# Optimization experiments

Hardware: AMD Instinct MI355X
Metric: run time of the kernel (lower is better)

The kernel has to match this reference:

```python
import jax, jax.numpy as jnp
import numpy as np

B, T, N, C, K = 32, 16, 512, 128, 2


def setup_inputs() -> dict:
    key = jax.random.key(0)
    k1, k2, k3 = jax.random.split(key, 3)
    x = jax.random.normal(k1, (B, T, N, C), dtype=jnp.float32)
    adj = jax.random.uniform(k2, (B, N, N), dtype=jnp.float32)
    lambdas = jnp.ones((K,), dtype=jnp.float32)           # raw lambda params (init 1.0)
    thetas = jax.random.uniform(k3, (K, C, C), dtype=jnp.float32)  # torch.rand init
    return {"x": x, "adj": adj, "lambdas": lambdas, "thetas": thetas}


def _akgcn_layer(x, adj, lam_raw, theta):
    # x: [B,T,N,C], adj: [B,N,N]
    lam = 1.0 + jax.nn.relu(lam_raw)  # actual lambda
    h = jnp.einsum('btnc,cd->btnd', x, theta)
    eye = jnp.eye(adj.shape[-1], dtype=adj.dtype)
    v = ((2.0 * lam - 2.0) / lam) * eye + (2.0 / lam) * adj   # [B,N,N]
    v = v / jnp.sum(v, axis=-1, keepdims=True)                 # row-normalize
    out = jnp.einsum('bnm,btmd->btnd', v, h)                   # vectorized over T
    return jax.nn.relu(out)


def reference(x, adj, lambdas, thetas):
    hid = x
    for k in range(K):  # small fixed layer count
        hid = _akgcn_layer(hid, adj, lambdas[k], thetas[k])
    return jax.nn.relu(x) + jax.nn.sigmoid(hid)
```

## Files before the change

kernel.cpp:

```cpp
#include <hip/hip_runtime.h>
#include <hip/hip_bf16.h>

#define BB 32
#define TT 16
#define NNODE 512
#define CC 128

typedef __attribute__((ext_vector_type(8))) short bf16x8;
typedef __attribute__((ext_vector_type(4))) short short4_t;
typedef __attribute__((ext_vector_type(4))) float f32x4;

__device__ __forceinline__ short f2bf(float f) {
    __hip_bfloat16 h = __float2bfloat16(f);
    return *reinterpret_cast<short*>(&h);
}

#define GLD16(g, l)                                                          \
    __builtin_amdgcn_global_load_lds(                                        \
        (const __attribute__((address_space(1))) unsigned int*)(g),          \
        (__attribute__((address_space(3))) unsigned int*)(l), 16, 0, 0)

__global__ void prep_adj2_kernel(const float* __restrict__ adj,
                                 const float* __restrict__ lambdas, int layer,
                                 short* __restrict__ Abf) {
    int gid = blockIdx.x * blockDim.x + threadIdx.x;
    int row = gid >> 6;
    int lane = gid & 63;
    int n = row & (NNODE - 1);
    const float* r = adj + (long)row * NNODE;
    float4 f0 = *(const float4*)(r + lane * 4);
    float4 f1 = *(const float4*)(r + 256 + lane * 4);
    float s = f0.x + f0.y + f0.z + f0.w + f1.x + f1.y + f1.z + f1.w;
#pragma unroll
    for (int o = 32; o; o >>= 1) s += __shfl_xor(s, o, 64);
    float lamm1 = fmaxf(lambdas[layer], 0.f);
    float inv = 1.f / (s + lamm1);
    float v[8] = {f0.x, f0.y, f0.z, f0.w, f1.x, f1.y, f1.z, f1.w};
#pragma unroll
    for (int j = 0; j < 8; ++j) v[j] *= inv;
    int d0 = n - lane * 4;
    if (d0 >= 0 && d0 < 4) v[d0] += lamm1 * inv;
    int d1 = n - 256 - lane * 4;
    if (d1 >= 0 && d1 < 4) v[4 + d1] += lamm1 * inv;
    short* o = Abf + (long)row * NNODE;
    short4_t s0 = {f2bf(v[0]), f2bf(v[1]), f2bf(v[2]), f2bf(v[3])};
    short4_t s1 = {f2bf(v[4]), f2bf(v[5]), f2bf(v[6]), f2bf(v[7])};
    *(short4_t*)(o + lane * 4) = s0;
    *(short4_t*)(o + 256 + lane * 4) = s1;
}

__global__ void prep_theta_kernel(const float* __restrict__ theta,
                                  short* __restrict__ thT) {
    int idx = blockIdx.x * 256 + threadIdx.x;
    int i = idx >> 7, k = idx & (CC - 1);
    thT[i * CC + k] = f2bf(theta[k * CC + i]);
}

__global__ __launch_bounds__(256) void gemm_theta_mfma(
    const float* __restrict__ X, const short* __restrict__ thT,
    short* __restrict__ Ht) {
    __shared__ short As[128 * 32];
    __shared__ short Bs[128 * 32];
    const int t = threadIdx.x;
    const long rowBase = (long)blockIdx.x * 128;
    const int w = t >> 6, ln = t & 63;
    const int lm = ln & 15, q = ln >> 4;
    const int wy = w >> 1, wx = w & 1;

    f32x4 acc[4][4] = {};

    const int rr = w * 32 + (ln >> 2);
    const int kc = (ln & 3) * 8;
    short* ldsB = Bs + w * 1024 + ln * 8;

    for (int k0 = 0; k0 < CC; k0 += 32) {
        __syncthreads();
        const short* gb = thT + rr * CC + k0 + kc;
        GLD16(gb, ldsB);
        GLD16(gb + 16 * CC, ldsB + 512);
#pragma unroll
        for (int i = 0; i < 4; ++i) {
            int v = i * 256 + t;
            int r = v >> 3, kq = v & 7;
            float4 f = *(const float4*)(X + (rowBase + r) * CC + k0 + kq * 4);
            short4_t s = {f2bf(f.x), f2bf(f.y), f2bf(f.z), f2bf(f.w)};
            *(short4_t*)(&As[r * 32 + kq * 4]) = s;
        }
        __syncthreads();

        bf16x8 a[4], b[4];
#pragma unroll
        for (int i = 0; i < 4; ++i)
            a[i] = *(const bf16x8*)(&As[(wy * 64 + i * 16 + lm) * 32 + q * 8]);
#pragma unroll
        for (int j = 0; j < 4; ++j)
            b[j] = *(const bf16x8*)(&Bs[(wx * 64 + j * 16 + lm) * 32 + q * 8]);
#pragma unroll
        for (int i = 0; i < 4; ++i)
#pragma unroll
            for (int j = 0; j < 4; ++j)
                acc[i][j] = __builtin_amdgcn_mfma_f32_16x16x32_bf16(
                    a[i], b[j], acc[i][j], 0, 0, 0);
    }

    const long bt = rowBase >> 9;
    const int mBase = (int)(rowBase & (NNODE - 1));
    short* Hb = Ht + bt * (long)(NNODE * CC);
#pragma unroll
    for (int i = 0; i < 4; ++i) {
        int m = mBase + wy * 64 + i * 16 + q * 4;
#pragma unroll
        for (int j = 0; j < 4; ++j) {
            int c = wx * 64 + j * 16 + lm;
            f32x4 v = acc[i][j];
            short4_t s = {f2bf(v[0]), f2bf(v[1]), f2bf(v[2]), f2bf(v[3])};
            *(short4_t*)(&Hb[(long)c * NNODE + m]) = s;
        }
    }
}

__global__ __launch_bounds__(256) void gemm_agg_theta(
    const short* __restrict__ Abf, const short* __restrict__ Ht1,
    const short* __restrict__ thT2, short* __restrict__ Ht2) {
    __shared__ short As[128 * 32];
    __shared__ short Bs[128 * 32];
    __shared__ short Ts[128][136];
    const int t = threadIdx.x;
    const int bt = blockIdx.y;
    const int n0 = blockIdx.x * 128;
    const short* Ab = Abf + (long)(bt >> 4) * NNODE * NNODE + (long)n0 * NNODE;
    const short* Hb = Ht1 + (long)bt * NNODE * CC;
    const int w = t >> 6, ln = t & 63;
    const int lm = ln & 15, q = ln >> 4;
    const int wy = w >> 1, wx = w & 1;

    f32x4 acc[4][4] = {};

    const int rr = w * 32 + (ln >> 2);
    const int kc = (ln & 3) * 8;
    short* ldsA = As + w * 1024 + ln * 8;
    short* ldsB = Bs + w * 1024 + ln * 8;

    for (int k0 = 0; k0 < NNODE; k0 += 32) {
        __syncthreads();
        const short* ga = Ab + (long)rr * NNODE + k0 + kc;
        const short* gb = Hb + (long)rr * NNODE + k0 + kc;
        GLD16(ga, ldsA);
        GLD16(ga + 16 * NNODE, ldsA + 512);
        GLD16(gb, ldsB);
        GLD16(gb + 16 * NNODE, ldsB + 512);
        __syncthreads();

        bf16x8 a[4], b[4];
#pragma unroll
        for (int i = 0; i < 4; ++i)
            a[i] = *(const bf16x8*)(&As[(wy * 64 + i * 16 + lm) * 32 + q * 8]);
#pragma unroll
        for (int j = 0; j < 4; ++j)
            b[j] = *(const bf16x8*)(&Bs[(wx * 64 + j * 16 + lm) * 32 + q * 8]);
#pragma unroll
        for (int i = 0; i < 4; ++i)
#pragma unroll
            for (int j = 0; j < 4; ++j)
                acc[i][j] = __builtin_amdgcn_mfma_f32_16x16x32_bf16(
                    a[i], b[j], acc[i][j], 0, 0, 0);
    }

#pragma unroll
    for (int i = 0; i < 4; ++i)
#pragma unroll
        for (int j = 0; j < 4; ++j)
#pragma unroll
            for (int r = 0; r < 4; ++r)
                Ts[wy * 64 + i * 16 + q * 4 + r][wx * 64 + j * 16 + lm] =
                    f2bf(fmaxf(acc[i][j][r], 0.f));

    f32x4 acc2[4][4] = {};
    for (int c0 = 0; c0 < CC; c0 += 32) {
        __syncthreads();
        const short* gb = thT2 + rr * CC + c0 + kc;
        GLD16(gb, ldsB);
        GLD16(gb + 16 * CC, ldsB + 512);
        __syncthreads();

        bf16x8 a[4], b[4];
#pragma unroll
        for (int i = 0; i < 4; ++i)
            a[i] = *(const bf16x8*)(&Ts[wy * 64 + i * 16 + lm][c0 + q * 8]);
#pragma unroll
        for (int j = 0; j < 4; ++j)
            b[j] = *(const bf16x8*)(&Bs[(wx * 64 + j * 16 + lm) * 32 + q * 8]);
#pragma unroll
        for (int i = 0; i < 4; ++i)
#pragma unroll
            for (int j = 0; j < 4; ++j)
                acc2[i][j] = __builtin_amdgcn_mfma_f32_16x16x32_bf16(
                    a[i], b[j], acc2[i][j], 0, 0, 0);
    }

    short* Hb2 = Ht2 + (long)bt * NNODE * CC;
#pragma unroll
    for (int i = 0; i < 4; ++i) {
        int m = n0 + wy * 64 + i * 16 + q * 4;
#pragma unroll
        for (int j = 0; j < 4; ++j) {
            int c = wx * 64 + j * 16 + lm;
            f32x4 v = acc2[i][j];
            short4_t sv = {f2bf(v[0]), f2bf(v[1]), f2bf(v[2]), f2bf(v[3])};
            *(short4_t*)(&Hb2[(long)c * NNODE + m]) = sv;
        }
    }
}

template <int FUSE>
__global__ __launch_bounds__(256) void gemm_agg_mfma(
    const short* __restrict__ Abf, const short* __restrict__ Ht,
    const float* __restrict__ x, float* __restrict__ Out) {
    __shared__ short As[128 * 32];
    __shared__ short Bs[128 * 32];
    const int t = threadIdx.x;
    const int bt = blockIdx.y;
    const int n0 = blockIdx.x * 128;
    const short* Ab = Abf + (long)(bt >> 4) * NNODE * NNODE + (long)n0 * NNODE;
    const short* Hb = Ht + (long)bt * NNODE * CC;
    const int w = t >> 6, ln = t & 63;
    const int lm = ln & 15, q = ln >> 4;
    const int wy = w >> 1, wx = w & 1;

    f32x4 acc[4][4] = {};

    const int rr = w * 32 + (ln >> 2);
    const int kc = (ln & 3) * 8;
    short* ldsA = As + w * 1024 + ln * 8;
    short* ldsB = Bs + w * 1024 + ln * 8;

    for (int k0 = 0; k0 < NNODE; k0 += 32) {
        __syncthreads();
        const short* ga = Ab + (long)rr * NNODE + k0 + kc;
        const short* gb = Hb + (long)rr * NNODE + k0 + kc;
        GLD16(ga, ldsA);
        GLD16(ga + 16 * NNODE, ldsA + 512);
        GLD16(gb, ldsB);
        GLD16(gb + 16 * NNODE, ldsB + 512);
        __syncthreads();

        bf16x8 a[4], b[4];
#pragma unroll
        for (int i = 0; i < 4; ++i)
            a[i] = *(const bf16x8*)(&As[(wy * 64 + i * 16 + lm) * 32 + q * 8]);
#pragma unroll
        for (int j = 0; j < 4; ++j)
            b[j] = *(const bf16x8*)(&Bs[(wx * 64 + j * 16 + lm) * 32 + q * 8]);
#pragma unroll
        for (int i = 0; i < 4; ++i)
#pragma unroll
            for (int j = 0; j < 4; ++j)
                acc[i][j] = __builtin_amdgcn_mfma_f32_16x16x32_bf16(
                    a[i], b[j], acc[i][j], 0, 0, 0);
    }

    const long obase = (long)bt * NNODE * CC;
#pragma unroll
    for (int i = 0; i < 4; ++i) {
        int n = n0 + wy * 64 + i * 16 + q * 4;
#pragma unroll
        for (int j = 0; j < 4; ++j) {
            int c = wx * 64 + j * 16 + lm;
#pragma unroll
            for (int r = 0; r < 4; ++r) {
                long idx = obase + (long)(n + r) * CC + c;
                float v = fmaxf(acc[i][j][r], 0.f);
                if (FUSE) {
                    Out[idx] = fmaxf(x[idx], 0.f) + 1.f / (1.f + __expf(-v));
                } else {
                    Out[idx] = v;
                }
            }
        }
    }
}

extern "C" void kernel_launch(void* const* d_in, const int* in_sizes, int n_in,
                              void* d_out, int out_size, void* d_ws,
                              size_t ws_size, hipStream_t stream) {
    const float* x = (const float*)d_in[0];
    const float* adj = (const float*)d_in[1];
    const float* lambdas = (const float*)d_in[2];
    const float* thetas = (const float*)d_in[3];
    float* out = (float*)d_out;

    short* Abf = (short*)d_ws;
    short* Ht2 = Abf + (long)BB * NNODE * NNODE;
    short* thT0 = Ht2 + (long)BB * TT * NNODE * CC;
    short* thT1 = thT0 + CC * CC;
    short* Ht1 = (short*)out;

    dim3 blk(256);
    dim3 g_agg(NNODE / 128, BB * TT);

    prep_adj2_kernel<<<4096, blk, 0, stream>>>(adj, lambdas, 0, Abf);
    prep_theta_kernel<<<64, blk, 0, stream>>>(thetas, thT0);
    prep_theta_kernel<<<64, blk, 0, stream>>>(thetas + CC * CC, thT1);

    gemm_theta_mfma<<<2048, blk, 0, stream>>>(x, thT0, Ht1);

    gemm_agg_theta<<<g_agg, blk, 0, stream>>>(Abf, Ht1, thT1, Ht2);

    prep_adj2_kernel<<<4096, blk, 0, stream>>>(adj, lambdas, 1, Abf);
    gemm_agg_mfma<1><<<g_agg, blk, 0, stream>>>(Abf, Ht2, x, out);
}
```

Baseline: 434.1 us.

## Double-buffer aggregation GEMMs, remap blocks, fuse prep kernels and preload theta

The aggregation GEMMs now double-buffer their LDS tiles, issuing the next k-slice's global-to-LDS loads before the current MFMAs so that load latency overlaps compute. They also use a 1D grid with a swizzled block-to-tile mapping meant to improve L2 reuse of the shared adjacency rows. The adjacency prep computes both layers' normalized matrices in one pass when the workspace is large enough, and the two theta transposes are merged into one launch. The theta GEMM keeps the whole theta in LDS and converts X straight into registers, and the second GEMM in gemm_agg_theta reads theta from global memory instead of staging it. The costs are higher LDS and workspace use, and a fallback path for when the workspace is too small.

After: 504.0 us. 1.16x slower.

```diff
diff --git a/kernel.cpp b/kernel.cpp
--- a/kernel.cpp
+++ b/kernel.cpp
@@ -20,9 +20,10 @@
         (const __attribute__((address_space(1))) unsigned int*)(g),          \
         (__attribute__((address_space(3))) unsigned int*)(l), 16, 0, 0)
 
-__global__ void prep_adj2_kernel(const float* __restrict__ adj,
-                                 const float* __restrict__ lambdas, int layer,
-                                 short* __restrict__ Abf) {
+__global__ void prep_adj_kernel(const float* __restrict__ adj,
+                                const float* __restrict__ lambdas, int layer0,
+                                short* __restrict__ Abf0,
+                                short* __restrict__ Abf1) {
     int gid = blockIdx.x * blockDim.x + threadIdx.x;
     int row = gid >> 6;
     int lane = gid & 63;
@@ -33,68 +34,76 @@
     float s = f0.x + f0.y + f0.z + f0.w + f1.x + f1.y + f1.z + f1.w;
 #pragma unroll
     for (int o = 32; o; o >>= 1) s += __shfl_xor(s, o, 64);
-    float lamm1 = fmaxf(lambdas[layer], 0.f);
-    float inv = 1.f / (s + lamm1);
-    float v[8] = {f0.x, f0.y, f0.z, f0.w, f1.x, f1.y, f1.z, f1.w};
-#pragma unroll
-    for (int j = 0; j < 8; ++j) v[j] *= inv;
+    float base[8] = {f0.x, f0.y, f0.z, f0.w, f1.x, f1.y, f1.z, f1.w};
     int d0 = n - lane * 4;
-    if (d0 >= 0 && d0 < 4) v[d0] += lamm1 * inv;
     int d1 = n - 256 - lane * 4;
-    if (d1 >= 0 && d1 < 4) v[4 + d1] += lamm1 * inv;
-    short* o = Abf + (long)row * NNODE;
-    short4_t s0 = {f2bf(v[0]), f2bf(v[1]), f2bf(v[2]), f2bf(v[3])};
-    short4_t s1 = {f2bf(v[4]), f2bf(v[5]), f2bf(v[6]), f2bf(v[7])};
-    *(short4_t*)(o + lane * 4) = s0;
-    *(short4_t*)(o + 256 + lane * 4) = s1;
-}
-
-__global__ void prep_theta_kernel(const float* __restrict__ theta,
+#pragma unroll
+    for (int l = 0; l < 2; ++l) {
+        short* dst = l ? Abf1 : Abf0;
+        if (dst == nullptr) continue;
+        float lamm1 = fmaxf(lambdas[layer0 + l], 0.f);
+        float inv = 1.f / (s + lamm1);
+        float v[8];
+#pragma unroll
+        for (int j = 0; j < 8; ++j) v[j] = base[j] * inv;
+        if (d0 >= 0 && d0 < 4) v[d0] += lamm1 * inv;
+        if (d1 >= 0 && d1 < 4) v[4 + d1] += lamm1 * inv;
+        short* o = dst + (long)row * NNODE;
+        short4_t s0 = {f2bf(v[0]), f2bf(v[1]), f2bf(v[2]), f2bf(v[3])};
+        short4_t s1 = {f2bf(v[4]), f2bf(v[5]), f2bf(v[6]), f2bf(v[7])};
+        *(short4_t*)(o + lane * 4) = s0;
+        *(short4_t*)(o + 256 + lane * 4) = s1;
+    }
+}
+
+__global__ void prep_theta_kernel(const float* __restrict__ thetas,
                                   short* __restrict__ thT) {
     int idx = blockIdx.x * 256 + threadIdx.x;
-    int i = idx >> 7, k = idx & (CC - 1);
-    thT[i * CC + k] = f2bf(theta[k * CC + i]);
+    int l = idx >> 14;
+    int r = idx & 16383;
+    int i = r >> 7, k = r & (CC - 1);
+    thT[l * CC * CC + i * CC + k] = f2bf(thetas[l * CC * CC + k * CC + i]);
 }
 
 __global__ __launch_bounds__(256) void gemm_theta_mfma(
     const float* __restrict__ X, const short* __restrict__ thT,
     short* __restrict__ Ht) {
-    __shared__ short As[128 * 32];
-    __shared__ short Bs[128 * 32];
+    __shared__ short Bs[128][136];
     const int t = threadIdx.x;
     const long rowBase = (long)blockIdx.x * 128;
     const int w = t >> 6, ln = t & 63;
     const int lm = ln & 15, q = ln >> 4;
     const int wy = w >> 1, wx = w & 1;
 
+    {
+        int row = t >> 1, half = (t & 1) * 64;
+        const short* src = thT + row * CC + half;
+#pragma unroll
+        for (int j = 0; j < 8; ++j)
+            *(bf16x8*)(&Bs[row][half + j * 8]) = *(const bf16x8*)(src + j * 8);
+    }
+    __syncthreads();
+
     f32x4 acc[4][4] = {};
-
-    const int rr = w * 32 + (ln >> 2);
-    const int kc = (ln & 3) * 8;
-    short* ldsB = Bs + w * 1024 + ln * 8;
-
+    const float* Xr = X + (rowBase + wy * 64 + lm) * CC;
+#pragma unroll
     for (int k0 = 0; k0 < CC; k0 += 32) {
-        __syncthreads();
-        const short* gb = thT + rr * CC + k0 + kc;
-        GLD16(gb, ldsB);
-        GLD16(gb + 16 * CC, ldsB + 512);
+        bf16x8 a[4], b[4];
 #pragma unroll
         for (int i = 0; i < 4; ++i) {
-            int v = i * 256 + t;
-            int r = v >> 3, kq = v & 7;
-            float4 f = *(const float4*)(X + (rowBase + r) * CC + k0 + kq * 4);
-            short4_t s = {f2bf(f.x), f2bf(f.y), f2bf(f.z), f2bf(f.w)};
-            *(short4_t*)(&As[r * 32 + kq * 4]) = s;
-        }
-        __syncthreads();
-
-        bf16x8 a[4], b[4];
-#pragma unroll
-        for (int i = 0; i < 4; ++i)
-            a[i] = *(const bf16x8*)(&As[(wy * 64 + i * 16 + lm) * 32 + q * 8]);
-#pragma unroll
-        for (int j = 0; j < 4; ++j)
-            b[j] = *(const bf16x8*)(&Bs[(wx * 64 + j * 16 + lm) * 32 + q * 8]);
+            const float* p = Xr + i * 16 * CC + k0 + q * 8;
+            float4 g0 = *(const float4*)(p);
+            float4 g1 = *(const float4*)(p + 4);
+            bf16x8 av;
+            av[0] = f2bf(g0.x); av[1] = f2bf(g0.y);
+            av[2] = f2bf(g0.z); av[3] = f2bf(g0.w);
+            av[4] = f2bf(g1.x); av[5] = f2bf(g1.y);
+            av[6] = f2bf(g1.z); av[7] = f2bf(g1.w);
+            a[i] = av;
+        }
+#pragma unroll
+        for (int j = 0; j < 4; ++j)
+            b[j] = *(const bf16x8*)(&Bs[wx * 64 + j * 16 + lm][k0 + q * 8]);
 #pragma unroll
         for (int i = 0; i < 4; ++i)
 #pragma unroll
@@ -113,8 +122,8 @@
         for (int j = 0; j < 4; ++j) {
             int c = wx * 64 + j * 16 + lm;
             f32x4 v = acc[i][j];
-            short4_t s = {f2bf(v[0]), f2bf(v[1]), f2bf(v[2]), f2bf(v[3])};
-            *(short4_t*)(&Hb[(long)c * NNODE + m]) = s;
+            short4_t sv = {f2bf(v[0]), f2bf(v[1]), f2bf(v[2]), f2bf(v[3])};
+            *(short4_t*)(&Hb[(long)c * NNODE + m]) = sv;
         }
     }
 }
@@ -122,12 +131,12 @@
 __global__ __launch_bounds__(256) void gemm_agg_theta(
     const short* __restrict__ Abf, const short* __restrict__ Ht1,
     const short* __restrict__ thT2, short* __restrict__ Ht2) {
-    __shared__ short As[128 * 32];
-    __shared__ short Bs[128 * 32];
-    __shared__ short Ts[128][136];
+    __shared__ short sh[17408];
     const int t = threadIdx.x;
-    const int bt = blockIdx.y;
-    const int n0 = blockIdx.x * 128;
+    const int bid = blockIdx.x;
+    const int wid = (bid & 7) * 256 + (bid >> 3);
+    const int bt = wid >> 2;
+    const int n0 = (wid & 3) * 128;
     const short* Ab = Abf + (long)(bt >> 4) * NNODE * NNODE + (long)n0 * NNODE;
     const short* Hb = Ht1 + (long)bt * NNODE * CC;
     const int w = t >> 6, ln = t & 63;
@@ -138,58 +147,65 @@
 
     const int rr = w * 32 + (ln >> 2);
     const int kc = (ln & 3) * 8;
-    short* ldsA = As + w * 1024 + ln * 8;
-    short* ldsB = Bs + w * 1024 + ln * 8;
-
+    const short* ga = Ab + (long)rr * NNODE + kc;
+    const short* gb = Hb + (long)rr * NNODE + kc;
+    const int lofs = w * 1024 + ln * 8;
+
+    GLD16(ga, sh + lofs);
+    GLD16(ga + 16 * NNODE, sh + lofs + 512);
+    GLD16(gb, sh + 8192 + lofs);
+    GLD16(gb + 16 * NNODE, sh + 8192 + lofs + 512);
+    __syncthreads();
+    int sel = 0;
     for (int k0 = 0; k0 < NNODE; k0 += 32) {
-        __syncthreads();
-        const short* ga = Ab + (long)rr * NNODE + k0 + kc;
-        const short* gb = Hb + (long)rr * NNODE + k0 + kc;
-        GLD16(ga, ldsA);
-        GLD16(ga + 16 * NNODE, ldsA + 512);
-        GLD16(gb, ldsB);
-        GLD16(gb + 16 * NNODE, ldsB + 512);
-        __syncthreads();
-
+        if (k0 + 32 < NNODE) {
+            const int no = (sel ^ 1) * 4096 + lofs;
+            GLD16(ga + k0 + 32, sh + no);
+            GLD16(ga + k0 + 32 + 16 * NNODE, sh + no + 512);
+            GLD16(gb + k0 + 32, sh + 8192 + no);
+            GLD16(gb + k0 + 32 + 16 * NNODE, sh + 8192 + no + 512);
+        }
+        const short* Ac = sh + sel * 4096;
+        const short* Bc = sh + 8192 + sel * 4096;
         bf16x8 a[4], b[4];
 #pragma unroll
         for (int i = 0; i < 4; ++i)
-            a[i] = *(const bf16x8*)(&As[(wy * 64 + i * 16 + lm) * 32 + q * 8]);
-#pragma unroll
-        for (int j = 0; j < 4; ++j)
-            b[j] = *(const bf16x8*)(&Bs[(wx * 64 + j * 16 + lm) * 32 + q * 8]);
+            a[i] = *(const bf16x8*)(Ac + (wy * 64 + i * 16 + lm) * 32 + q * 8);
+#pragma unroll
+        for (int j = 0; j < 4; ++j)
+            b[j] = *(const bf16x8*)(Bc + (wx * 64 + j * 16 + lm) * 32 + q * 8);
 #pragma unroll
         for (int i = 0; i < 4; ++i)
 #pragma unroll
             for (int j = 0; j < 4; ++j)
                 acc[i][j] = __builtin_amdgcn_mfma_f32_16x16x32_bf16(
                     a[i], b[j], acc[i][j], 0, 0, 0);
-    }
-
+        __syncthreads();
+        sel ^= 1;
+    }
+
+    short(*Ts)[136] = (short(*)[136])sh;
 #pragma unroll
     for (int i = 0; i < 4; ++i)
 #pragma unroll
         for (int j = 0; j < 4; ++j)
 #pragma unroll
-            for (int r = 0; r < 4; ++r)
-                Ts[wy * 64 + i * 16 + q * 4 + r][wx * 64 + j * 16 + lm] =
-                    f2bf(fmaxf(acc[i][j][r], 0.f));
+            for (int r2 = 0; r2 < 4; ++r2)
+                Ts[wy * 64 + i * 16 + q * 4 + r2][wx * 64 + j * 16 + lm] =
+                    f2bf(fmaxf(acc[i][j][r2], 0.f));
+    __syncthreads();
 
     f32x4 acc2[4][4] = {};
+#pragma unroll
     for (int c0 = 0; c0 < CC; c0 += 32) {
-        __syncthreads();
-        const short* gb = thT2 + rr * CC + c0 + kc;
-        GLD16(gb, ldsB);
-        GLD16(gb + 16 * CC, ldsB + 512);
-        __syncthreads();
-
         bf16x8 a[4], b[4];
 #pragma unroll
         for (int i = 0; i < 4; ++i)
             a[i] = *(const bf16x8*)(&Ts[wy * 64 + i * 16 + lm][c0 + q * 8]);
 #pragma unroll
         for (int j = 0; j < 4; ++j)
-            b[j] = *(const bf16x8*)(&Bs[(wx * 64 + j * 16 + lm) * 32 + q * 8]);
+            b[j] = *(const bf16x8*)(thT2 + (wx * 64 + j * 16 + lm) * CC + c0 +
+                                    q * 8);
 #pragma unroll
         for (int i = 0; i < 4; ++i)
 #pragma unroll
@@ -212,15 +228,15 @@
     }
 }
 
-template <int FUSE>
 __global__ __launch_bounds__(256) void gemm_agg_mfma(
     const short* __restrict__ Abf, const short* __restrict__ Ht,
     const float* __restrict__ x, float* __restrict__ Out) {
-    __shared__ short As[128 * 32];
-    __shared__ short Bs[128 * 32];
+    __shared__ short sh[16384];
     const int t = threadIdx.x;
-    const int bt = blockIdx.y;
-    const int n0 = blockIdx.x * 128;
+    const int bid = blockIdx.x;
+    const int wid = (bid & 7) * 256 + (bid >> 3);
+    const int bt = wid >> 2;
+    const int n0 = (wid & 3) * 128;
     const short* Ab = Abf + (long)(bt >> 4) * NNODE * NNODE + (long)n0 * NNODE;
     const short* Hb = Ht + (long)bt * NNODE * CC;
     const int w = t >> 6, ln = t & 63;
@@ -231,32 +247,41 @@
 
     const int rr = w * 32 + (ln >> 2);
     const int kc = (ln & 3) * 8;
-    short* ldsA = As + w * 1024 + ln * 8;
-    short* ldsB = Bs + w * 1024 + ln * 8;
-
+    const short* ga = Ab + (long)rr * NNODE + kc;
+    const short* gb = Hb + (long)rr * NNODE + kc;
+    const int lofs = w * 1024 + ln * 8;
+
+    GLD16(ga, sh + lofs);
+    GLD16(ga + 16 * NNODE, sh + lofs + 512);
+    GLD16(gb, sh + 8192 + lofs);
+    GLD16(gb + 16 * NNODE, sh + 8192 + lofs + 512);
+    __syncthreads();
+    int sel = 0;
     for (int k0 = 0; k0 < NNODE; k0 += 32) {
-        __syncthreads();
-        const short* ga = Ab + (long)rr * NNODE + k0 + kc;
-        const short* gb = Hb + (long)rr * NNODE + k0 + kc;
-        GLD16(ga, ldsA);
-        GLD16(ga + 16 * NNODE, ldsA + 512);
-        GLD16(gb, ldsB);
-        GLD16(gb + 16 * NNODE, ldsB + 512);
-        __syncthreads();
-
+        if (k0 + 32 < NNODE) {
+            const int no = (sel ^ 1) * 4096 + lofs;
+            GLD16(ga + k0 + 32, sh + no);
+            GLD16(ga + k0 + 32 + 16 * NNODE, sh + no + 512);
+            GLD16(gb + k0 + 32, sh + 8192 + no);
+            GLD16(gb + k0 + 32 + 16 * NNODE, sh + 8192 + no + 512);
+        }
+        const short* Ac = sh + sel * 4096;
+        const short* Bc = sh + 8192 + sel * 4096;
         bf16x8 a[4], b[4];
 #pragma unroll
         for (int i = 0; i < 4; ++i)
-            a[i] = *(const bf16x8*)(&As[(wy * 64 + i * 16 + lm) * 32 + q * 8]);
-#pragma unroll
-        for (int j = 0; j < 4; ++j)
-            b[j] = *(const bf16x8*)(&Bs[(wx * 64 + j * 16 + lm) * 32 + q * 8]);
+            a[i] = *(const bf16x8*)(Ac + (wy * 64 + i * 16 + lm) * 32 + q * 8);
+#pragma unroll
+        for (int j = 0; j < 4; ++j)
+            b[j] = *(const bf16x8*)(Bc + (wx * 64 + j * 16 + lm) * 32 + q * 8);
 #pragma unroll
         for (int i = 0; i < 4; ++i)
 #pragma unroll
             for (int j = 0; j < 4; ++j)
                 acc[i][j] = __builtin_amdgcn_mfma_f32_16x16x32_bf16(
                     a[i], b[j], acc[i][j], 0, 0, 0);
+        __syncthreads();
+        sel ^= 1;
     }
 
     const long obase = (long)bt * NNODE * CC;
@@ -267,14 +292,10 @@
         for (int j = 0; j < 4; ++j) {
             int c = wx * 64 + j * 16 + lm;
 #pragma unroll
-            for (int r = 0; r < 4; ++r) {
-                long idx = obase + (long)(n + r) * CC + c;
-                float v = fmaxf(acc[i][j][r], 0.f);
-                if (FUSE) {
-                    Out[idx] = fmaxf(x[idx], 0.f) + 1.f / (1.f + __expf(-v));
-                } else {
-                    Out[idx] = v;
-                }
+            for (int r2 = 0; r2 < 4; ++r2) {
+                long idx = obase + (long)(n + r2) * CC + c;
+                float v = fmaxf(acc[i][j][r2], 0.f);
+                Out[idx] = fmaxf(x[idx], 0.f) + 1.f / (1.f + __expf(-v));
             }
         }
     }
@@ -289,23 +310,34 @@
     const float* thetas = (const float*)d_in[3];
     float* out = (float*)d_out;
 
-    short* Abf = (short*)d_ws;
-    short* Ht2 = Abf + (long)BB * NNODE * NNODE;
-    short* thT0 = Ht2 + (long)BB * TT * NNODE * CC;
+    const long abf_elems = (long)BB * NNODE * NNODE;
+    const long ht_elems = (long)BB * TT * NNODE * CC;
+    const bool two =
+        ws_size >= (size_t)(2 * abf_elems + ht_elems + 2 * CC * CC) * 2;
+
+    short* Abf0 = (short*)d_ws;
+    short* Abf1 = two ? Abf0 + abf_elems : Abf0;
+    short* Ht2 = Abf1 + abf_elems;
+    short* thT0 = Ht2 + ht_elems;
     short* thT1 = thT0 + CC * CC;
     short* Ht1 = (short*)out;
 
     dim3 blk(256);
-    dim3 g_agg(NNODE / 128, BB * TT);
-
-    prep_adj2_kernel<<<4096, blk, 0, stream>>>(adj, lambdas, 0, Abf);
-    prep_theta_kernel<<<64, blk, 0, stream>>>(thetas, thT0);
-    prep_theta_kernel<<<64, blk, 0, stream>>>(thetas + CC * CC, thT1);
-
-    gemm_theta_mfma<<<2048, blk, 0, stream>>>(x, thT0, Ht1);
-
-    gemm_agg_theta<<<g_agg, blk, 0, stream>>>(Abf, Ht1, thT1, Ht2);
-
-    prep_adj2_kernel<<<4096, blk, 0, stream>>>(adj, lambdas, 1, Abf);
-    gemm_agg_mfma<1><<<g_agg, blk, 0, stream>>>(Abf, Ht2, x, out);
-}
+
+    if (two) {
+        prep_adj_kernel<<<4096, blk, 0, stream>>>(adj, lambdas, 0, Abf0, Abf1);
+        prep_theta_kernel<<<128, blk, 0, stream>>>(thetas, thT0);
+        gemm_theta_mfma<<<2048, blk, 0, stream>>>(x, thT0, Ht1);
+        gemm_agg_theta<<<2048, blk, 0, stream>>>(Abf0, Ht1, thT1, Ht2);
+        gemm_agg_mfma<<<2048, blk, 0, stream>>>(Abf1, Ht2, x, out);
+    } else {
+        prep_adj_kernel<<<4096, blk, 0, stream>>>(adj, lambdas, 0, Abf0,
+                                                  nullptr);
+        prep_theta_kernel<<<128, blk, 0, stream>>>(thetas, thT0);
+        gemm_theta_mfma<<<2048, blk, 0, stream>>>(x, thT0, Ht1);
+        gemm_agg_theta<<<2048, blk, 0, stream>>>(Abf0, Ht1, thT1, Ht2);
+        prep_adj_kernel<<<4096, blk, 0, stream>>>(adj, lambdas, 1, Abf0,
+                                                  nullptr);
+        gemm_agg_mfma<<<2048, blk, 0, stream>>>(Abf0, Ht2, x, out);
+    }
+}
```
